# Performance work log

Measured on AMD Instinct MI355X. Metric: run time of the kernel, lower is better.

Reference implementation:

```python
import jax, jax.numpy as jnp
import numpy as np

N_NODES = 50000
N_EDGES = 800000
D = 64           # node feature / hidden dim for all 5 GCN layers
NUM_GRAPHS = 512
FINAL_NEURON = 128
OUT_DIM = 1
NUM_LAYERS = 5


def setup_inputs() -> dict:
    key = jax.random.key(0)
    ks = jax.random.split(key, 20)
    inp = {}
    inp["x"] = jax.random.normal(ks[0], (N_NODES, D), dtype=jnp.float32)
    inp["edge_index"] = jax.random.randint(ks[1], (2, N_EDGES), 0, N_NODES)
    inp["batch"] = jnp.sort(jax.random.randint(ks[2], (N_NODES,), 0, NUM_GRAPHS))
    # GCNConv weights (Glorot-ish) and biases for 5 layers, all D->D
    for i in range(NUM_LAYERS):
        inp[f"W{i+1}"] = jax.random.normal(ks[3 + i], (D, D), dtype=jnp.float32) / np.sqrt(D)
        inp[f"b{i+1}"] = jnp.zeros((D,), dtype=jnp.float32)
    inp["fc1_W"] = jax.random.normal(ks[10], (D, FINAL_NEURON), dtype=jnp.float32) / np.sqrt(D)
    inp["fc1_b"] = jnp.zeros((FINAL_NEURON,), dtype=jnp.float32)
    inp["fc2_W"] = jax.random.normal(ks[11], (FINAL_NEURON, OUT_DIM), dtype=jnp.float32) / np.sqrt(FINAL_NEURON)
    inp["fc2_b"] = jnp.zeros((OUT_DIM,), dtype=jnp.float32)
    return inp


def _gcn_conv(h, src, dst, dinv, W, b):
    # PyG GCNConv: x' = D^{-1/2} (A + I) D^{-1/2} (h W) + b, deg includes self-loop
    hw = h @ W                                           # [N, D_out]
    norm_e = dinv[src] * dinv[dst]                       # [E]
    msg = hw[src] * norm_e[:, None]                      # gather + scale
    agg = jax.ops.segment_sum(msg, dst, num_segments=h.shape[0])
    agg = agg + (dinv * dinv)[:, None] * hw              # self-loop contribution
    return agg + b


def reference(x, edge_index, batch, W1, b1, W2, b2, W3, b3, W4, b4, W5, b5,
              fc1_W, fc1_b, fc2_W, fc2_b):
    src, dst = edge_index[0], edge_index[1]
    n = x.shape[0]
    # degree on A + I (in-degree at dst, plus 1 self-loop)
    deg = jax.ops.segment_sum(jnp.ones(src.shape[0], x.dtype), dst, num_segments=n) + 1.0
    dinv = jax.lax.rsqrt(deg)
    h = x
    for W, b in ((W1, b1), (W2, b2), (W3, b3), (W4, b4), (W5, b5)):
        h = jax.nn.relu(_gcn_conv(h, src, dst, dinv, W, b))
    # global_add_pool readout over graph ids
    g = jax.ops.segment_sum(h, batch, num_segments=NUM_GRAPHS)   # [G, D]
    g = jax.nn.relu(g @ fc1_W + fc1_b)
    return g @ fc2_W + fc2_b                                     # [G, 1]
```

## Files before the change

kernel.cpp:

```cpp
#include <hip/hip_runtime.h>
#include <hip/hip_fp16.h>

#define N_NODES 50000
#define N_EDGES 800000
#define D 64
#define NUM_GRAPHS 512
#define FINAL_NEURON 128
#define SCAN_NB ((N_NODES + 255) / 256)

#define BN 16
#define NB_GEMM (N_NODES / BN)
#define NB_EDGE ((N_EDGES + 255) / 256)
#define ZS 72
#define WS 72
#define WELEM (D * WS)

typedef unsigned short ushort_t;
typedef _Float16 f16;
typedef __attribute__((ext_vector_type(4))) _Float16 f16x4;
typedef __attribute__((ext_vector_type(8))) _Float16 f16x8;
typedef __attribute__((ext_vector_type(4))) float f32x4;

struct WPtrs { const float* w[5]; };

__device__ __forceinline__ float2 h2f(unsigned v) {
    __half2 h = *reinterpret_cast<__half2*>(&v);
    return __half22float2(h);
}

__device__ __forceinline__ void acc_add8(float4& a0, float4& a1, uint4 u) {
    float2 p;
    p = h2f(u.x); a0.x += p.x; a0.y += p.y;
    p = h2f(u.y); a0.z += p.x; a0.w += p.y;
    p = h2f(u.z); a1.x += p.x; a1.y += p.y;
    p = h2f(u.w); a1.z += p.x; a1.w += p.y;
}

__global__ void k_zero_prep(int* cnt, WPtrs wp, f16* __restrict__ whi, f16* __restrict__ wlo) {
    int b = blockIdx.x;
    if (b < SCAN_NB) {
        int i = b * 256 + threadIdx.x;
        if (i < N_NODES) cnt[i] = 0;
        return;
    }
    int l = b - SCAN_NB;
    const float* W = wp.w[l];
    f16* hi = whi + l * WELEM;
    f16* lo = wlo + l * WELEM;
    for (int idx = threadIdx.x; idx < D * D; idx += 256) {
        int k = idx >> 6, j = idx & 63;
        float w = W[idx];
        f16 h = (f16)w;
        hi[j * WS + k] = h;
        lo[j * WS + k] = (f16)(w - (float)h);
    }
}

__global__ void k_hist(const int* __restrict__ dst, int* cnt, ushort_t* __restrict__ epos) {
    int e = blockIdx.x * blockDim.x + threadIdx.x;
    if (e < N_EDGES) epos[e] = (ushort_t)atomicAdd(&cnt[dst[e]], 1);
}

__global__ void k_blocksum(const int* __restrict__ cnt, int* __restrict__ bsum,
                           float* __restrict__ dinv, float* __restrict__ g) {
    __shared__ int sdata[256];
    int t = threadIdx.x;
    int i = blockIdx.x * 256 + t;
    int v = (i < N_NODES) ? cnt[i] : 0;
    if (i < N_NODES) dinv[i] = rsqrtf((float)v + 1.0f);
    if (i < NUM_GRAPHS * D) g[i] = 0.f;
    sdata[t] = v;
    __syncthreads();
    for (int s = 128; s > 0; s >>= 1) {
        if (t < s) sdata[t] += sdata[t + s];
        __syncthreads();
    }
    if (t == 0) bsum[blockIdx.x] = sdata[0];
}

__global__ void k_scanbsum(const int* __restrict__ bsum, int* __restrict__ boff) {
    __shared__ int buf[256];
    int t = threadIdx.x;
    int v = (t < SCAN_NB) ? bsum[t] : 0;
    buf[t] = v;
    __syncthreads();
    for (int off = 1; off < 256; off <<= 1) {
        int a = (t >= off) ? buf[t - off] : 0;
        __syncthreads();
        buf[t] += a;
        __syncthreads();
    }
    if (t < SCAN_NB) boff[t] = buf[t] - v;
}

__global__ void k_localscan(const int* __restrict__ cnt, const int* __restrict__ boff,
                            int* __restrict__ row) {
    __shared__ int buf[256];
    int t = threadIdx.x;
    int i = blockIdx.x * 256 + t;
    int v = (i < N_NODES) ? cnt[i] : 0;
    buf[t] = v;
    __syncthreads();
    for (int off = 1; off < 256; off <<= 1) {
        int a = (t >= off) ? buf[t - off] : 0;
        __syncthreads();
        buf[t] += a;
        __syncthreads();
    }
    if (i < N_NODES) row[i] = boff[blockIdx.x] + buf[t] - v;
    if (i == 0) row[N_NODES] = N_EDGES;
}

__device__ __forceinline__ void stage_w_lds(const f16* __restrict__ whi_g,
                                            const f16* __restrict__ wlo_g,
                                            f16* WhiT, f16* WloT, int t) {
    const uint4* sh = (const uint4*)whi_g;
    const uint4* sl = (const uint4*)wlo_g;
    uint4* dh = (uint4*)WhiT;
    uint4* dl = (uint4*)WloT;
#pragma unroll 3
    for (int i = 0; i < 3; ++i) {
        int idx = t + i * 256;
        if (idx < WELEM / 8) { dh[idx] = sh[idx]; dl[idx] = sl[idx]; }
    }
}

__device__ __forceinline__ void gather_node16(const int* __restrict__ row,
                                              const ushort_t* __restrict__ esrc,
                                              const uint4* __restrict__ hp,
                                              int n, int g, int q, float4& a0, float4& a1) {
    int e = row[n] + g, e1 = row[n + 1];
    if (g == 0) acc_add8(a0, a1, hp[(size_t)n * 8 + q]);
    int i0 = __builtin_nontemporal_load(esrc + e);
    int i1 = __builtin_nontemporal_load(esrc + e + 2);
    int i2 = __builtin_nontemporal_load(esrc + e + 4);
    int i3 = __builtin_nontemporal_load(esrc + e + 6);
    while (e + 6 < e1) {
        uint4 u0 = hp[(size_t)i0 * 8 + q];
        uint4 u1 = hp[(size_t)i1 * 8 + q];
        uint4 u2 = hp[(size_t)i2 * 8 + q];
        uint4 u3 = hp[(size_t)i3 * 8 + q];
        e += 8;
        i0 = __builtin_nontemporal_load(esrc + e);
        i1 = __builtin_nontemporal_load(esrc + e + 2);
        i2 = __builtin_nontemporal_load(esrc + e + 4);
        i3 = __builtin_nontemporal_load(esrc + e + 6);
        acc_add8(a0, a1, u0); acc_add8(a0, a1, u1);
        acc_add8(a0, a1, u2); acc_add8(a0, a1, u3);
    }
    for (; e < e1; e += 2) {
        int s = __builtin_nontemporal_load(esrc + e);
        acc_add8(a0, a1, hp[(size_t)s * 8 + q]);
    }
}

__device__ __forceinline__ void gemm_16x64(f16* zsh, const f16* WhiT, const f16* WloT,
                                           const float* dinvsh, int t) {
    int w = t >> 6, l = t & 63;
    int cb = w * 16;
    int lr = l & 15, lg = l >> 4;
    f32x4 acc = {0.f, 0.f, 0.f, 0.f};
    f16x8 a0  = *(const f16x8*)&zsh[lr * ZS + lg * 8];
    f16x8 a1  = *(const f16x8*)&zsh[lr * ZS + 32 + lg * 8];
    f16x8 bh0 = *(const f16x8*)&WhiT[(cb + lr) * WS + lg * 8];
    f16x8 bl0 = *(const f16x8*)&WloT[(cb + lr) * WS + lg * 8];
    f16x8 bh1 = *(const f16x8*)&WhiT[(cb + lr) * WS + 32 + lg * 8];
    f16x8 bl1 = *(const f16x8*)&WloT[(cb + lr) * WS + 32 + lg * 8];
    acc = __builtin_amdgcn_mfma_f32_16x16x32_f16(a0, bh0, acc, 0, 0, 0);
    acc = __builtin_amdgcn_mfma_f32_16x16x32_f16(a0, bl0, acc, 0, 0, 0);
    acc = __builtin_amdgcn_mfma_f32_16x16x32_f16(a1, bh1, acc, 0, 0, 0);
    acc = __builtin_amdgcn_mfma_f32_16x16x32_f16(a1, bl1, acc, 0, 0, 0);
    __syncthreads();
#pragma unroll
    for (int r = 0; r < 4; ++r) {
        int rrow = lg * 4 + r;
        float s = dinvsh[rrow];
        zsh[rrow * ZS + cb + lr] = (f16)(acc[r] * s);
    }
}

__global__ __launch_bounds__(256, 6)
void k_transform0(const float* __restrict__ x, const float* __restrict__ dinv,
                  const f16* __restrict__ whi_g, const f16* __restrict__ wlo_g,
                  __half* __restrict__ hout,
                  const int* __restrict__ src, const int* __restrict__ dst,
                  const int* __restrict__ row, const ushort_t* __restrict__ epos,
                  ushort_t* __restrict__ esrc) {
    int t = threadIdx.x;
    if (blockIdx.x >= NB_GEMM) {
        int e = (blockIdx.x - NB_GEMM) * 256 + t;
        if (e < N_EDGES) esrc[row[dst[e]] + (int)epos[e]] = (ushort_t)src[e];
        return;
    }
    __shared__ __attribute__((aligned(16))) f16 WhiT[WELEM];
    __shared__ __attribute__((aligned(16))) f16 WloT[WELEM];
    __shared__ __attribute__((aligned(16))) f16 zsh[BN * ZS];
    __shared__ float dinvsh[BN];
    int base = blockIdx.x * BN;
    stage_w_lds(whi_g, wlo_g, WhiT, WloT, t);
    if (t < BN) dinvsh[t] = dinv[base + t];

    int nl = t >> 4, c4 = t & 15;
    float4 xv = ((const float4*)x)[(size_t)(base + nl) * 16 + c4];
    f16x4 zv = {(f16)xv.x, (f16)xv.y, (f16)xv.z, (f16)xv.w};
    *(f16x4*)&zsh[nl * ZS + c4 * 4] = zv;
    __syncthreads();
    gemm_16x64(zsh, WhiT, WloT, dinvsh, t);
    __syncthreads();
    if (t < 128) {
        int n2 = t >> 3, q = t & 7;
        uint4 o = *(const uint4*)&zsh[n2 * ZS + q * 8];
        ((uint4*)hout)[(size_t)(base + n2) * 8 + q] = o;
    }
}

__global__ __launch_bounds__(256, 6)
void k_layer(const int* __restrict__ row, const ushort_t* __restrict__ esrc,
             const __half* __restrict__ hin, const float* __restrict__ dinv,
             const float* __restrict__ bias,
             const f16* __restrict__ whi_g, const f16* __restrict__ wlo_g,
             __half* __restrict__ hout) {
    __shared__ __attribute__((aligned(16))) f16 WhiT[WELEM];
    __shared__ __attribute__((aligned(16))) f16 WloT[WELEM];
    __shared__ __attribute__((aligned(16))) f16 zsh[BN * ZS];
    __shared__ float dinvsh[BN];
    int t = threadIdx.x;
    int base = blockIdx.x * BN;
    stage_w_lds(whi_g, wlo_g, WhiT, WloT, t);
    if (t < BN) dinvsh[t] = dinv[base + t];

    int nl = t >> 4, m = t & 15, g = m >> 3, q = m & 7;
    int n = base + nl;
    float4 a0 = {0,0,0,0}, a1 = {0,0,0,0};
    gather_node16(row, esrc, (const uint4*)hin, n, g, q, a0, a1);
    a0.x += __shfl_xor(a0.x, 8); a0.y += __shfl_xor(a0.y, 8);
    a0.z += __shfl_xor(a0.z, 8); a0.w += __shfl_xor(a0.w, 8);
    a1.x += __shfl_xor(a1.x, 8); a1.y += __shfl_xor(a1.y, 8);
    a1.z += __shfl_xor(a1.z, 8); a1.w += __shfl_xor(a1.w, 8);
    float s = dinv[n];
    float4 b0 = ((const float4*)bias)[2 * q];
    float4 b1 = ((const float4*)bias)[2 * q + 1];
    if (g == 0) {
        f16x8 zv;
        zv[0] = (f16)fmaxf(a0.x * s + b0.x, 0.f);
        zv[1] = (f16)fmaxf(a0.y * s + b0.y, 0.f);
        zv[2] = (f16)fmaxf(a0.z * s + b0.z, 0.f);
        zv[3] = (f16)fmaxf(a0.w * s + b0.w, 0.f);
        zv[4] = (f16)fmaxf(a1.x * s + b1.x, 0.f);
        zv[5] = (f16)fmaxf(a1.y * s + b1.y, 0.f);
        zv[6] = (f16)fmaxf(a1.z * s + b1.z, 0.f);
        zv[7] = (f16)fmaxf(a1.w * s + b1.w, 0.f);
        *(f16x8*)&zsh[nl * ZS + q * 8] = zv;
    }
    __syncthreads();
    gemm_16x64(zsh, WhiT, WloT, dinvsh, t);
    __syncthreads();
    if (t < 128) {
        int n2 = t >> 3, q2 = t & 7;
        uint4 o = *(const uint4*)&zsh[n2 * ZS + q2 * 8];
        ((uint4*)hout)[(size_t)(base + n2) * 8 + q2] = o;
    }
}

__global__ __launch_bounds__(256, 6)
void k_layer_pool(const int* __restrict__ row, const ushort_t* __restrict__ esrc,
                  const __half* __restrict__ hin, const float* __restrict__ dinv,
                  const float* __restrict__ bias, const int* __restrict__ batch,
                  float* __restrict__ g) {
    __shared__ float zf[BN * 68];
    __shared__ int bsh[BN];
    int t = threadIdx.x;
    int base = blockIdx.x * BN;
    if (t < BN) bsh[t] = batch[base + t];

    int nl = t >> 4, m = t & 15, g2 = m >> 3, q = m & 7;
    int n = base + nl;
    float4 a0 = {0,0,0,0}, a1 = {0,0,0,0};
    gather_node16(row, esrc, (const uint4*)hin, n, g2, q, a0, a1);
    a0.x += __shfl_xor(a0.x, 8); a0.y += __shfl_xor(a0.y, 8);
    a0.z += __shfl_xor(a0.z, 8); a0.w += __shfl_xor(a0.w, 8);
    a1.x += __shfl_xor(a1.x, 8); a1.y += __shfl_xor(a1.y, 8);
    a1.z += __shfl_xor(a1.z, 8); a1.w += __shfl_xor(a1.w, 8);
    float s = dinv[n];
    float4 b0 = ((const float4*)bias)[2 * q];
    float4 b1 = ((const float4*)bias)[2 * q + 1];
    if (g2 == 0) {
        float4 r0, r1;
        r0.x = fmaxf(a0.x * s + b0.x, 0.f);
        r0.y = fmaxf(a0.y * s + b0.y, 0.f);
        r0.z = fmaxf(a0.z * s + b0.z, 0.f);
        r0.w = fmaxf(a0.w * s + b0.w, 0.f);
        r1.x = fmaxf(a1.x * s + b1.x, 0.f);
        r1.y = fmaxf(a1.y * s + b1.y, 0.f);
        r1.z = fmaxf(a1.z * s + b1.z, 0.f);
        r1.w = fmaxf(a1.w * s + b1.w, 0.f);
        *(float4*)&zf[nl * 68 + q * 8]     = r0;
        *(float4*)&zf[nl * 68 + q * 8 + 4] = r1;
    }
    __syncthreads();
    int f = t & 63, grp = t >> 6;
    int n0 = grp * 4;
    int cur = bsh[n0];
    float acc = 0.f;
#pragma unroll
    for (int k2 = 0; k2 < 4; ++k2) {
        int bb = bsh[n0 + k2];
        if (bb != cur) { atomicAdd(&g[cur * D + f], acc); acc = 0.f; cur = bb; }
        acc += zf[(n0 + k2) * 68 + f];
    }
    atomicAdd(&g[cur * D + f], acc);
}

__global__ void k_mlp(const float* __restrict__ g, const float* __restrict__ W1,
                      const float* __restrict__ b1, const float* __restrict__ W2,
                      const float* __restrict__ b2, float* __restrict__ out) {
    __shared__ float red[FINAL_NEURON];
    int row = blockIdx.x;
    int j = threadIdx.x;
    float acc = 0.f;
#pragma unroll
    for (int k = 0; k < D; ++k) acc += g[row * D + k] * W1[k * FINAL_NEURON + j];
    acc = fmaxf(acc + b1[j], 0.f);
    red[j] = acc * W2[j];
    __syncthreads();
    for (int s = 64; s > 0; s >>= 1) {
        if (j < s) red[j] += red[j + s];
        __syncthreads();
    }
    if (j == 0) out[row] = red[0] + b2[0];
}

extern "C" void kernel_launch(void* const* d_in, const int* in_sizes, int n_in,
                              void* d_out, int out_size, void* d_ws, size_t ws_size,
                              hipStream_t stream) {
    const float* x     = (const float*)d_in[0];
    const int*   ei    = (const int*)d_in[1];
    const int*   src   = ei;
    const int*   dst   = ei + N_EDGES;
    const int*   batch = (const int*)d_in[2];
    WPtrs wp;
    wp.w[0] = (const float*)d_in[3];  wp.w[1] = (const float*)d_in[5];
    wp.w[2] = (const float*)d_in[7];  wp.w[3] = (const float*)d_in[9];
    wp.w[4] = (const float*)d_in[11];
    const float* b[5]  = {(const float*)d_in[4], (const float*)d_in[6], (const float*)d_in[8],
                          (const float*)d_in[10], (const float*)d_in[12]};
    const float* fc1W  = (const float*)d_in[13];
    const float* fc1b  = (const float*)d_in[14];
    const float* fc2W  = (const float*)d_in[15];
    const float* fc2b  = (const float*)d_in[16];
    float* out = (float*)d_out;

    __half*   yA   = (__half*)d_ws;
    __half*   yB   = yA + (size_t)N_NODES * D;
    f16*      whiG = (f16*)(yB + (size_t)N_NODES * D);
    f16*      wloG = whiG + 5 * WELEM;
    float*    g    = (float*)(wloG + 5 * WELEM);
    float*    dinv = g + NUM_GRAPHS * D;
    int*      cnt  = (int*)(dinv + N_NODES);
    int*      row  = cnt + N_NODES;
    int*      bsum = row + N_NODES + 1;
    int*      boff = bsum + 256;
    ushort_t* epos = (ushort_t*)(boff + 256);
    ushort_t* esrc = epos + N_EDGES;

    k_zero_prep<<<SCAN_NB + 5, 256, 0, stream>>>(cnt, wp, whiG, wloG);
    k_hist<<<(N_EDGES + 255) / 256, 256, 0, stream>>>(dst, cnt, epos);
    k_blocksum<<<SCAN_NB, 256, 0, stream>>>(cnt, bsum, dinv, g);
    k_scanbsum<<<1, 256, 0, stream>>>(bsum, boff);
    k_localscan<<<SCAN_NB, 256, 0, stream>>>(cnt, boff, row);

    k_transform0<<<NB_GEMM + NB_EDGE, 256, 0, stream>>>(x, dinv, whiG, wloG, yA,
                                                        src, dst, row, epos, esrc);

    k_layer<<<NB_GEMM, 256, 0, stream>>>(row, esrc, yA, dinv, b[0],
                                         whiG + 1 * WELEM, wloG + 1 * WELEM, yB);
    k_layer<<<NB_GEMM, 256, 0, stream>>>(row, esrc, yB, dinv, b[1],
                                         whiG + 2 * WELEM, wloG + 2 * WELEM, yA);
    k_layer<<<NB_GEMM, 256, 0, stream>>>(row, esrc, yA, dinv, b[2],
                                         whiG + 3 * WELEM, wloG + 3 * WELEM, yB);
    k_layer<<<NB_GEMM, 256, 0, stream>>>(row, esrc, yB, dinv, b[3],
                                         whiG + 4 * WELEM, wloG + 4 * WELEM, yA);

    k_layer_pool<<<NB_GEMM, 256, 0, stream>>>(row, esrc, yA, dinv, b[4], batch, g);

    k_mlp<<<NUM_GRAPHS, FINAL_NEURON, 0, stream>>>(g, fc1W, fc1b, fc2W, fc2b, out);
}
```

Baseline: 262.8 us.

## Load GEMM weights directly into registers and split edge gather into contiguous halves

Stops staging the split-precision weight matrices in shared memory each block. Each lane now loads its MFMA B-fragments straight from global memory, which cuts LDS usage and lets launch bounds request more blocks per CU. The per-node edge gather changes from interleaved stride-2 ownership to two contiguous halves, with an 8-wide unrolled loop and a 4/2/1 remainder tail. This aims for more memory-level parallelism and less index-load overhead. The risk is higher register pressure and repeated global/L2 weight reads per block. NB_EDGE also changes to truncating division, which is only exact because the edge count divides by 256.

```diff
diff --git a/kernel.cpp b/kernel.cpp
--- a/kernel.cpp
+++ b/kernel.cpp
@@ -10,7 +10,7 @@
 
 #define BN 16
 #define NB_GEMM (N_NODES / BN)
-#define NB_EDGE ((N_EDGES + 255) / 256)
+#define NB_EDGE (N_EDGES / 256)
 #define ZS 72
 #define WS 72
 #define WELEM (D * WS)
@@ -111,61 +111,75 @@
     if (i == 0) row[N_NODES] = N_EDGES;
 }
 
-__device__ __forceinline__ void stage_w_lds(const f16* __restrict__ whi_g,
-                                            const f16* __restrict__ wlo_g,
-                                            f16* WhiT, f16* WloT, int t) {
-    const uint4* sh = (const uint4*)whi_g;
-    const uint4* sl = (const uint4*)wlo_g;
-    uint4* dh = (uint4*)WhiT;
-    uint4* dl = (uint4*)WloT;
-#pragma unroll 3
-    for (int i = 0; i < 3; ++i) {
-        int idx = t + i * 256;
-        if (idx < WELEM / 8) { dh[idx] = sh[idx]; dl[idx] = sl[idx]; }
-    }
-}
-
-__device__ __forceinline__ void gather_node16(const int* __restrict__ row,
-                                              const ushort_t* __restrict__ esrc,
-                                              const uint4* __restrict__ hp,
-                                              int n, int g, int q, float4& a0, float4& a1) {
-    int e = row[n] + g, e1 = row[n + 1];
-    if (g == 0) acc_add8(a0, a1, hp[(size_t)n * 8 + q]);
-    int i0 = __builtin_nontemporal_load(esrc + e);
-    int i1 = __builtin_nontemporal_load(esrc + e + 2);
-    int i2 = __builtin_nontemporal_load(esrc + e + 4);
-    int i3 = __builtin_nontemporal_load(esrc + e + 6);
-    while (e + 6 < e1) {
-        uint4 u0 = hp[(size_t)i0 * 8 + q];
-        uint4 u1 = hp[(size_t)i1 * 8 + q];
-        uint4 u2 = hp[(size_t)i2 * 8 + q];
-        uint4 u3 = hp[(size_t)i3 * 8 + q];
-        e += 8;
-        i0 = __builtin_nontemporal_load(esrc + e);
-        i1 = __builtin_nontemporal_load(esrc + e + 2);
-        i2 = __builtin_nontemporal_load(esrc + e + 4);
-        i3 = __builtin_nontemporal_load(esrc + e + 6);
+__device__ __forceinline__ void gather_half(const int* __restrict__ row,
+                                            const ushort_t* __restrict__ esrc,
+                                            const uint4* __restrict__ hp,
+                                            int n, int g, int q,
+                                            float4& a0, float4& a1) {
+    int e0 = row[n], e1 = row[n + 1];
+    int len = e1 - e0;
+    int h0 = (len + 1) >> 1;
+    int e  = g ? (e0 + h0) : e0;
+    int eg = g ? e1 : (e0 + h0);
+    if (g) acc_add8(a0, a1, hp[(size_t)n * 8 + q]);
+    int m = eg - e;
+    int i0, i1, i2, i3, i4, i5, i6, i7;
+    if (m >= 8) {
+        i0 = esrc[e];     i1 = esrc[e + 1]; i2 = esrc[e + 2]; i3 = esrc[e + 3];
+        i4 = esrc[e + 4]; i5 = esrc[e + 5]; i6 = esrc[e + 6]; i7 = esrc[e + 7];
+        for (;;) {
+            uint4 u0 = hp[(size_t)i0 * 8 + q], u1 = hp[(size_t)i1 * 8 + q];
+            uint4 u2 = hp[(size_t)i2 * 8 + q], u3 = hp[(size_t)i3 * 8 + q];
+            uint4 u4 = hp[(size_t)i4 * 8 + q], u5 = hp[(size_t)i5 * 8 + q];
+            uint4 u6 = hp[(size_t)i6 * 8 + q], u7 = hp[(size_t)i7 * 8 + q];
+            e += 8; m -= 8;
+            i0 = esrc[e];     i1 = esrc[e + 1]; i2 = esrc[e + 2]; i3 = esrc[e + 3];
+            i4 = esrc[e + 4]; i5 = esrc[e + 5]; i6 = esrc[e + 6]; i7 = esrc[e + 7];
+            acc_add8(a0, a1, u0); acc_add8(a0, a1, u1);
+            acc_add8(a0, a1, u2); acc_add8(a0, a1, u3);
+            acc_add8(a0, a1, u4); acc_add8(a0, a1, u5);
+            acc_add8(a0, a1, u6); acc_add8(a0, a1, u7);
+            if (m < 8) break;
+        }
+    } else {
+        if (m <= 0) return;
+        i0 = esrc[e];     i1 = esrc[e + 1]; i2 = esrc[e + 2]; i3 = esrc[e + 3];
+        i4 = esrc[e + 4]; i5 = esrc[e + 5]; i6 = esrc[e + 6]; i7 = esrc[e + 7];
+    }
+    if (m & 4) {
+        uint4 u0 = hp[(size_t)i0 * 8 + q], u1 = hp[(size_t)i1 * 8 + q];
+        uint4 u2 = hp[(size_t)i2 * 8 + q], u3 = hp[(size_t)i3 * 8 + q];
         acc_add8(a0, a1, u0); acc_add8(a0, a1, u1);
         acc_add8(a0, a1, u2); acc_add8(a0, a1, u3);
-    }
-    for (; e < e1; e += 2) {
-        int s = __builtin_nontemporal_load(esrc + e);
-        acc_add8(a0, a1, hp[(size_t)s * 8 + q]);
-    }
-}
-
-__device__ __forceinline__ void gemm_16x64(f16* zsh, const f16* WhiT, const f16* WloT,
-                                           const float* dinvsh, int t) {
+        i0 = i4; i1 = i5; i2 = i6; i3 = i7;
+    }
+    if (m & 2) {
+        uint4 u0 = hp[(size_t)i0 * 8 + q], u1 = hp[(size_t)i1 * 8 + q];
+        acc_add8(a0, a1, u0); acc_add8(a0, a1, u1);
+        i0 = i2; i1 = i3;
+    }
+    if (m & 1) {
+        uint4 u0 = hp[(size_t)i0 * 8 + q];
+        acc_add8(a0, a1, u0);
+    }
+}
+
+__device__ __forceinline__ void gemm_16x64_reg(f16* zsh,
+                                               const f16* __restrict__ whi_g,
+                                               const f16* __restrict__ wlo_g,
+                                               const float* dinvsh, int t) {
     int w = t >> 6, l = t & 63;
     int cb = w * 16;
     int lr = l & 15, lg = l >> 4;
+    const f16* bhp = &whi_g[(cb + lr) * WS + lg * 8];
+    const f16* blp = &wlo_g[(cb + lr) * WS + lg * 8];
+    f16x8 bh0 = *(const f16x8*)bhp;
+    f16x8 bl0 = *(const f16x8*)blp;
+    f16x8 bh1 = *(const f16x8*)(bhp + 32);
+    f16x8 bl1 = *(const f16x8*)(blp + 32);
     f32x4 acc = {0.f, 0.f, 0.f, 0.f};
-    f16x8 a0  = *(const f16x8*)&zsh[lr * ZS + lg * 8];
-    f16x8 a1  = *(const f16x8*)&zsh[lr * ZS + 32 + lg * 8];
-    f16x8 bh0 = *(const f16x8*)&WhiT[(cb + lr) * WS + lg * 8];
-    f16x8 bl0 = *(const f16x8*)&WloT[(cb + lr) * WS + lg * 8];
-    f16x8 bh1 = *(const f16x8*)&WhiT[(cb + lr) * WS + 32 + lg * 8];
-    f16x8 bl1 = *(const f16x8*)&WloT[(cb + lr) * WS + 32 + lg * 8];
+    f16x8 a0 = *(const f16x8*)&zsh[lr * ZS + lg * 8];
+    f16x8 a1 = *(const f16x8*)&zsh[lr * ZS + 32 + lg * 8];
     acc = __builtin_amdgcn_mfma_f32_16x16x32_f16(a0, bh0, acc, 0, 0, 0);
     acc = __builtin_amdgcn_mfma_f32_16x16x32_f16(a0, bl0, acc, 0, 0, 0);
     acc = __builtin_amdgcn_mfma_f32_16x16x32_f16(a1, bh1, acc, 0, 0, 0);
@@ -179,7 +193,7 @@
     }
 }
 
-__global__ __launch_bounds__(256, 6)
+__global__ __launch_bounds__(256, 8)
 void k_transform0(const float* __restrict__ x, const float* __restrict__ dinv,
                   const f16* __restrict__ whi_g, const f16* __restrict__ wlo_g,
                   __half* __restrict__ hout,
@@ -192,12 +206,9 @@
         if (e < N_EDGES) esrc[row[dst[e]] + (int)epos[e]] = (ushort_t)src[e];
         return;
     }
-    __shared__ __attribute__((aligned(16))) f16 WhiT[WELEM];
-    __shared__ __attribute__((aligned(16))) f16 WloT[WELEM];
     __shared__ __attribute__((aligned(16))) f16 zsh[BN * ZS];
     __shared__ float dinvsh[BN];
     int base = blockIdx.x * BN;
-    stage_w_lds(whi_g, wlo_g, WhiT, WloT, t);
     if (t < BN) dinvsh[t] = dinv[base + t];
 
     int nl = t >> 4, c4 = t & 15;
@@ -205,7 +216,7 @@
     f16x4 zv = {(f16)xv.x, (f16)xv.y, (f16)xv.z, (f16)xv.w};
     *(f16x4*)&zsh[nl * ZS + c4 * 4] = zv;
     __syncthreads();
-    gemm_16x64(zsh, WhiT, WloT, dinvsh, t);
+    gemm_16x64_reg(zsh, whi_g, wlo_g, dinvsh, t);
     __syncthreads();
     if (t < 128) {
         int n2 = t >> 3, q = t & 7;
@@ -214,25 +225,22 @@
     }
 }
 
-__global__ __launch_bounds__(256, 6)
+__global__ __launch_bounds__(256, 7)
 void k_layer(const int* __restrict__ row, const ushort_t* __restrict__ esrc,
              const __half* __restrict__ hin, const float* __restrict__ dinv,
              const float* __restrict__ bias,
              const f16* __restrict__ whi_g, const f16* __restrict__ wlo_g,
              __half* __restrict__ hout) {
-    __shared__ __attribute__((aligned(16))) f16 WhiT[WELEM];
-    __shared__ __attribute__((aligned(16))) f16 WloT[WELEM];
     __shared__ __attribute__((aligned(16))) f16 zsh[BN * ZS];
     __shared__ float dinvsh[BN];
     int t = threadIdx.x;
     int base = blockIdx.x * BN;
-    stage_w_lds(whi_g, wlo_g, WhiT, WloT, t);
     if (t < BN) dinvsh[t] = dinv[base + t];
 
     int nl = t >> 4, m = t & 15, g = m >> 3, q = m & 7;
     int n = base + nl;
     float4 a0 = {0,0,0,0}, a1 = {0,0,0,0};
-    gather_node16(row, esrc, (const uint4*)hin, n, g, q, a0, a1);
+    gather_half(row, esrc, (const uint4*)hin, n, g, q, a0, a1);
     a0.x += __shfl_xor(a0.x, 8); a0.y += __shfl_xor(a0.y, 8);
     a0.z += __shfl_xor(a0.z, 8); a0.w += __shfl_xor(a0.w, 8);
     a1.x += __shfl_xor(a1.x, 8); a1.y += __shfl_xor(a1.y, 8);
@@ -253,7 +261,7 @@
         *(f16x8*)&zsh[nl * ZS + q * 8] = zv;
     }
     __syncthreads();
-    gemm_16x64(zsh, WhiT, WloT, dinvsh, t);
+    gemm_16x64_reg(zsh, whi_g, wlo_g, dinvsh, t);
     __syncthreads();
     if (t < 128) {
         int n2 = t >> 3, q2 = t & 7;
@@ -262,7 +270,7 @@
     }
 }
 
-__global__ __launch_bounds__(256, 6)
+__global__ __launch_bounds__(256, 7)
 void k_layer_pool(const int* __restrict__ row, const ushort_t* __restrict__ esrc,
                   const __half* __restrict__ hin, const float* __restrict__ dinv,
                   const float* __restrict__ bias, const int* __restrict__ batch,
@@ -276,7 +284,7 @@
     int nl = t >> 4, m = t & 15, g2 = m >> 3, q = m & 7;
     int n = base + nl;
     float4 a0 = {0,0,0,0}, a1 = {0,0,0,0};
-    gather_node16(row, esrc, (const uint4*)hin, n, g2, q, a0, a1);
+    gather_half(row, esrc, (const uint4*)hin, n, g2, q, a0, a1);
     a0.x += __shfl_xor(a0.x, 8); a0.y += __shfl_xor(a0.y, 8);
     a0.z += __shfl_xor(a0.z, 8); a0.w += __shfl_xor(a0.w, 8);
     a1.x += __shfl_xor(a1.x, 8); a1.y += __shfl_xor(a1.y, 8);
```

After: 242.6 us. 1.08x faster.
